# Performance work log

Measured on AMD Instinct MI355X. Metric: run time of the kernel, lower is better.

## Reference

```python
import jax, jax.numpy as jnp
import numpy as np

B, C_IN, T = 8, 1024, 4096
VQ_C, CODEBOOK, DS = 1024, 2048, 2


def setup_inputs() -> dict:
    key = jax.random.key(0)
    ks = jax.random.split(key, 6)
    return {
        "x": jax.random.normal(ks[0], (B, C_IN, T), jnp.float32),
        "x_mask": jnp.ones((B, 1, T), jnp.float32),
        "w_in": jax.random.normal(ks[1], (VQ_C, C_IN, DS), jnp.float32) * 0.02,
        "b_in": jnp.zeros((VQ_C,), jnp.float32),
        "embed": jax.random.normal(ks[2], (CODEBOOK, VQ_C), jnp.float32),
        "w_out": jax.random.normal(ks[3], (C_IN, VQ_C), jnp.float32) * 0.02,
        "b_out": jnp.zeros((C_IN,), jnp.float32),
    }


def reference(x, x_mask, w_in, b_in, embed, w_out, b_out):
    x_len = x.shape[2]
    ds = w_in.shape[-1]
    pad = (-x_len) % ds  # static under jit
    if pad:
        x = jnp.pad(x, ((0, 0), (0, 0), (0, pad)))
        x_mask = jnp.pad(x_mask, ((0, 0), (0, 0), (0, pad)))
    b, cin, tp = x.shape
    # conv_in: Conv1d(k=ds, stride=ds) == non-overlapping window contraction
    h = jnp.einsum('bcls,ocs->bol', x.reshape(b, cin, tp // ds, ds), w_in) + b_in[None, :, None]  # [B, D, L]
    tokens = h.transpose(0, 2, 1)  # [B, L, D]
    # euclidean codebook: ||t - e||^2 expanded (stable for argmin)
    d2 = (jnp.sum(tokens * tokens, -1, keepdims=True)
          - 2.0 * jnp.einsum('bld,nd->bln', tokens, embed)
          + jnp.sum(embed * embed, -1)[None, None, :])  # [B, L, N]
    idx = jnp.argmin(d2, axis=-1)  # [B, L]
    q = embed[idx]  # gather -> [B, L, D]
    # commitment loss (training-mode math; EMA codebook -> embed not a grad path)
    commit_loss = jnp.mean((jax.lax.stop_gradient(q) - tokens) ** 2)
    # straight-through estimator
    q_st = tokens + jax.lax.stop_gradient(q - tokens)
    q_cf = q_st.transpose(0, 2, 1)  # [B, D, L]
    # conv_out: nearest upsample x ds, then 1x1 conv
    up = jnp.repeat(q_cf, ds, axis=2)  # [B, D, Tp]
    out = jnp.einsum('bct,oc->bot', up, w_out) + b_out[None, :, None]
    out = out * x_mask
    return out[:, :, :x_len], commit_loss
```

## Files before the change

kernel.cpp:

```cpp
#include <hip/hip_runtime.h>

typedef _Float16 half8 __attribute__((ext_vector_type(8)));
typedef float f32x4 __attribute__((ext_vector_type(4)));

static constexpr int D = 1024;
static constexpr int NCODE = 2048;
static constexpr int MTOK = 16384;
static constexpr int KIN = 2048;
static constexpr int TLEN = 4096;
static constexpr int CAP = 2048;
#define TAU 0.4f

__device__ __forceinline__ void gload16(const void* g, void* l) {
  __builtin_amdgcn_global_load_lds(
      (const __attribute__((address_space(1))) void*)g,
      (__attribute__((address_space(3))) void*)l, 16, 0, 0);
}

#define SBAR()   asm volatile("s_barrier" ::: "memory")
#define WAITV4() asm volatile("s_waitcnt vmcnt(4)" ::: "memory")
#define WAITV0() asm volatile("s_waitcnt vmcnt(0)" ::: "memory")

__device__ __forceinline__ float key_to_f32(unsigned u) {
  unsigned bits = (u & 0x80000000u) ? (u & 0x7FFFFFFFu) : ~u;
  return __uint_as_float(bits);
}
__device__ __forceinline__ unsigned f32_to_key(float f) {
  unsigned ub = __float_as_uint(f);
  return (ub & 0x80000000u) ? ~ub : (ub | 0x80000000u);
}

__global__ __launch_bounds__(256) void k_pack_x(const float* __restrict__ x,
                                                _Float16* __restrict__ xh,
                                                _Float16* __restrict__ xl) {
  __shared__ float lds[32][65];
  const int tt0 = blockIdx.x * 64;
  const int cc0 = blockIdx.y * 32;
  const int b = blockIdx.z;
  const float* xb = x + ((size_t)b * D + cc0) * TLEN + tt0;
#pragma unroll
  for (int i = 0; i < 8; ++i) {
    int idx = threadIdx.x + i * 256;
    lds[idx >> 6][idx & 63] = xb[(size_t)(idx >> 6) * TLEN + (idx & 63)];
  }
  __syncthreads();
  const size_t mrow0 = (size_t)b * 2048 + (tt0 >> 1);
  const int r = threadIdx.x >> 3;
  const int g = threadIdx.x & 7;
  half8 vh, vl;
#pragma unroll
  for (int j = 0; j < 8; ++j) {
    int kk = g * 8 + j;
    float v = lds[kk >> 1][2 * r + (kk & 1)];
    _Float16 h = (_Float16)v;
    vh[j] = h;
    vl[j] = (_Float16)(v - (float)h);
  }
  size_t off = (mrow0 + r) * (size_t)KIN + (size_t)cc0 * 2 + g * 8;
  *(half8*)(xh + off) = vh;
  *(half8*)(xl + off) = vl;
}

__global__ __launch_bounds__(256) void k_split(const float* __restrict__ s,
                                               _Float16* __restrict__ hi,
                                               _Float16* __restrict__ lo, int n) {
  int i = blockIdx.x * 256 + threadIdx.x;
  if (i < n) {
    float v = s[i];
    _Float16 h = (_Float16)v;
    hi[i] = h;
    lo[i] = (_Float16)(v - (float)h);
  }
}

__global__ __launch_bounds__(256) void k_e2(const float* __restrict__ embed,
                                            float* __restrict__ e2c,
                                            int* __restrict__ counter,
                                            double* __restrict__ lossacc) {
  if (blockIdx.x == 0 && threadIdx.x == 0) { counter[0] = 0; lossacc[0] = 0.0; }
  int row = blockIdx.x * 4 + (threadIdx.x >> 6);
  int lane = threadIdx.x & 63;
  const float* er = embed + (size_t)row * D;
  double s = 0.0;
  for (int i = lane; i < D; i += 64) { double v = er[i]; s += v * v; }
#pragma unroll
  for (int mk = 1; mk < 64; mk <<= 1) s += __shfl_xor(s, mk, 64);
  if (lane == 0) e2c[row] = (float)(s - 1024.0);
}

template <int KDIM, int LOG_GX, int MODE>
__global__ __launch_bounds__(512, 2) void k_gemm_hh(
    const _Float16* __restrict__ Ah_, const _Float16* __restrict__ Bh_,
    const float* __restrict__ vec,
    _Float16* __restrict__ outh,
    unsigned long long* __restrict__ skKey, float* __restrict__ skSnd) {
  __shared__ _Float16 lds[3 * 16384];
  const int nwg = gridDim.x, bid = blockIdx.x, q = nwg >> 3;
  const int b2 = (bid & 7) * q + (bid >> 3);
  const int nb = b2 & ((1 << LOG_GX) - 1);
  const int n0 = nb * 256, m0 = (b2 >> LOG_GX) * 256;
  const int tid = threadIdx.x, lane = tid & 63, w = tid >> 6;
  const int wr = w >> 2, wc = w & 3, lr = lane & 15, lk = lane >> 4;
  constexpr int NT = KDIM / 32;
  const int cswz8 = (((lane & 3) ^ ((lane >> 3) & 3))) * 8;
  const int rswz8 = (lk ^ ((lr >> 1) & 3)) * 8;

  f32x4 acc[8][4] = {};

  auto stage = [&](int t, int c) {
    char* sb = (char*)(lds + c * 16384);
    const int k0 = t * 32;
    const int r0 = (w * 64 + lane) >> 2;
    gload16(Ah_ + (size_t)(m0 + r0) * KDIM + k0 + cswz8, sb + w * 1024);
    gload16(Ah_ + (size_t)(m0 + 128 + r0) * KDIM + k0 + cswz8, sb + w * 1024 + 8192);
    gload16(Bh_ + (size_t)(n0 + r0) * KDIM + k0 + cswz8, sb + 16384 + w * 1024);
    gload16(Bh_ + (size_t)(n0 + 128 + r0) * KDIM + k0 + cswz8, sb + 16384 + w * 1024 + 8192);
  };

  stage(0, 0);
  stage(1, 1);
  WAITV4();
  SBAR();

  int c0 = 0, c1 = 1, c2 = 2;
  for (int t = 0; t < NT; ++t) {
    const bool st = (t + 2) < NT;
    if (st) stage(t + 2, c2);
    const _Float16* sb = lds + c0 * 16384;
    half8 ah[8], bh[4];
#pragma unroll
    for (int f = 0; f < 8; ++f)
      ah[f] = *(const half8*)(sb + (wr * 128 + f * 16 + lr) * 32 + rswz8);
#pragma unroll
    for (int f = 0; f < 4; ++f)
      bh[f] = *(const half8*)(sb + 8192 + (wc * 64 + f * 16 + lr) * 32 + rswz8);
    __builtin_amdgcn_s_setprio(1);
#pragma unroll
    for (int fm = 0; fm < 8; ++fm)
#pragma unroll
      for (int fn = 0; fn < 4; ++fn)
        acc[fm][fn] = __builtin_amdgcn_mfma_f32_16x16x32_f16(ah[fm], bh[fn], acc[fm][fn], 0, 0, 0);
    __builtin_amdgcn_s_setprio(0);
    if (st) { WAITV4(); } else if (t + 1 < NT) { WAITV0(); }
    SBAR();
    int tmp = c0; c0 = c1; c1 = c2; c2 = tmp;
  }

  if constexpr (MODE == 0) {
#pragma unroll
    for (int fm = 0; fm < 8; ++fm) {
#pragma unroll
      for (int j = 0; j < 4; ++j) {
        int row = wr * 128 + fm * 16 + lk * 4 + j;
        size_t m = (size_t)m0 + row;
#pragma unroll
        for (int fn = 0; fn < 4; ++fn) {
          int col = n0 + wc * 64 + fn * 16 + lr;
          outh[m * (size_t)D + col] = (_Float16)(acc[fm][fn][j] + vec[col]);
        }
      }
    }
  } else {
#pragma unroll
    for (int fm = 0; fm < 8; ++fm) {
#pragma unroll
      for (int j = 0; j < 4; ++j) {
        int row = wr * 128 + fm * 16 + lk * 4 + j;
        size_t m = (size_t)m0 + row;
        float b1 = 3.4e38f, bb2 = 3.4e38f;
        int i1 = 0x7FFFFFFF;
#pragma unroll
        for (int fn = 0; fn < 4; ++fn) {
          int col = n0 + wc * 64 + fn * 16 + lr;
          float mv = vec[col] - 2.0f * acc[fm][fn][j];
          if (mv < b1) { bb2 = b1; b1 = mv; i1 = col; }
          else if (mv < bb2) { bb2 = mv; }
        }
#pragma unroll
        for (int mk = 1; mk < 16; mk <<= 1) {
          float ob1 = __shfl_xor(b1, mk, 64);
          float ob2 = __shfl_xor(bb2, mk, 64);
          int oi = __shfl_xor(i1, mk, 64);
          if (ob1 < b1) { bb2 = fminf(b1, ob2); b1 = ob1; i1 = oi; }
          else { bb2 = fminf(bb2, ob1); }
        }
        if (lr == 0) {
          unsigned long long key = ((unsigned long long)f32_to_key(b1) << 32) | (unsigned)i1;
          skKey[m * 32 + nb * 4 + wc] = key;
          skSnd[m * 32 + nb * 4 + wc] = bb2;
        }
      }
    }
  }
}

__global__ __launch_bounds__(256) void k_t2(const _Float16* __restrict__ tokh,
                                            float* __restrict__ t2) {
  const int w = threadIdx.x >> 6, lane = threadIdx.x & 63;
  const int row = blockIdx.x * 4 + w;
  const _Float16* tr = tokh + (size_t)row * D + lane * 16;
  float s = 0.f;
#pragma unroll
  for (int v = 0; v < 2; ++v) {
    half8 h = *(const half8*)(tr + v * 8);
#pragma unroll
    for (int j = 0; j < 8; ++j) { float f = (float)h[j]; s += f * f; }
  }
#pragma unroll
  for (int mk = 1; mk < 64; mk <<= 1) s += __shfl_xor(s, mk, 64);
  if (lane == 0) t2[row] = s;
}

__global__ __launch_bounds__(256) void k_flag(const unsigned long long* __restrict__ skKey,
                                              const float* __restrict__ skSnd,
                                              unsigned long long* __restrict__ keys,
                                              unsigned long long* __restrict__ keys2,
                                              int* __restrict__ list, int* __restrict__ counter) {
  int m = blockIdx.x * 256 + threadIdx.x;
  keys2[m] = ~0ull;
  unsigned long long best = ~0ull;
  int bsl = 0;
#pragma unroll
  for (int sl = 0; sl < 32; ++sl) {
    unsigned long long k = skKey[(size_t)m * 32 + sl];
    if (k < best) { best = k; bsl = sl; }
  }
  float b1 = key_to_f32((unsigned)(best >> 32));
  float second = skSnd[(size_t)m * 32 + bsl];
#pragma unroll
  for (int sl = 0; sl < 32; ++sl) {
    if (sl != bsl) second = fminf(second, key_to_f32((unsigned)(skKey[(size_t)m * 32 + sl] >> 32)));
  }
  keys[m] = best;
  if (second - b1 < TAU) {
    int p = atomicAdd(counter, 1);
    if (p < CAP) list[p] = m;
  }
}

__global__ __launch_bounds__(256) void k_tok_fix(
    const _Float16* __restrict__ xh, const _Float16* __restrict__ xl,
    const _Float16* __restrict__ wh, const _Float16* __restrict__ wl,
    const float* __restrict__ b_in, const int* __restrict__ list,
    const int* __restrict__ counter,
    _Float16* __restrict__ tokh2, _Float16* __restrict__ tokl2) {
  const int count = min(counter[0], CAP);
  const int m0 = blockIdx.y * 128;
  if (m0 >= count) return;
  __shared__ _Float16 sAh[128 * 32], sAl[128 * 32], sBh[128 * 32], sBl[128 * 32];
  const int n0 = blockIdx.x * 128;
  const int tid = threadIdx.x, lane = tid & 63, w = tid >> 6;
  const int wr = w >> 1, wc = w & 1, lr = lane & 15, lk = lane >> 4;
  f32x4 acc[4][4] = {};

  const int g0 = w * 128 + lane, g1 = g0 + 64;
  const int rA0 = g0 >> 2, cA0 = g0 & 3, rA1 = g1 >> 2, cA1 = g1 & 3;
  const int lb0 = (w * 128) * 16, lb1 = (w * 128 + 64) * 16;
  const int tk0 = list[min(m0 + rA0, count - 1)];
  const int tk1 = list[min(m0 + rA1, count - 1)];

  for (int kt = 0; kt < KIN / 32; ++kt) {
    const int k0 = kt * 32;
    gload16(xh + (size_t)tk0 * KIN + k0 + cA0 * 8, (char*)sAh + lb0);
    gload16(xh + (size_t)tk1 * KIN + k0 + cA1 * 8, (char*)sAh + lb1);
    gload16(xl + (size_t)tk0 * KIN + k0 + cA0 * 8, (char*)sAl + lb0);
    gload16(xl + (size_t)tk1 * KIN + k0 + cA1 * 8, (char*)sAl + lb1);
    gload16(wh + (size_t)(n0 + rA0) * KIN + k0 + cA0 * 8, (char*)sBh + lb0);
    gload16(wh + (size_t)(n0 + rA1) * KIN + k0 + cA1 * 8, (char*)sBh + lb1);
    gload16(wl + (size_t)(n0 + rA0) * KIN + k0 + cA0 * 8, (char*)sBl + lb0);
    gload16(wl + (size_t)(n0 + rA1) * KIN + k0 + cA1 * 8, (char*)sBl + lb1);
    __syncthreads();
    half8 ah[4], al2[4], bh[4], bl2[4];
#pragma unroll
    for (int f = 0; f < 4; ++f) {
      ah[f]  = *(const half8*)(sAh + (wr * 64 + f * 16 + lr) * 32 + lk * 8);
      al2[f] = *(const half8*)(sAl + (wr * 64 + f * 16 + lr) * 32 + lk * 8);
      bh[f]  = *(const half8*)(sBh + (wc * 64 + f * 16 + lr) * 32 + lk * 8);
      bl2[f] = *(const half8*)(sBl + (wc * 64 + f * 16 + lr) * 32 + lk * 8);
    }
#pragma unroll
    for (int fm = 0; fm < 4; ++fm)
#pragma unroll
      for (int fn = 0; fn < 4; ++fn) {
        acc[fm][fn] = __builtin_amdgcn_mfma_f32_16x16x32_f16(ah[fm], bh[fn], acc[fm][fn], 0, 0, 0);
        acc[fm][fn] = __builtin_amdgcn_mfma_f32_16x16x32_f16(ah[fm], bl2[fn], acc[fm][fn], 0, 0, 0);
        acc[fm][fn] = __builtin_amdgcn_mfma_f32_16x16x32_f16(al2[fm], bh[fn], acc[fm][fn], 0, 0, 0);
      }
    __syncthreads();
  }
#pragma unroll
  for (int fm = 0; fm < 4; ++fm) {
#pragma unroll
    for (int j = 0; j < 4; ++j) {
      int row = wr * 64 + fm * 16 + lk * 4 + j;
      if (m0 + row >= count) continue;
#pragma unroll
      for (int fn = 0; fn < 4; ++fn) {
        int col = n0 + wc * 64 + fn * 16 + lr;
        float v = acc[fm][fn][j] + b_in[col];
        _Float16 h = (_Float16)v;
        tokh2[(size_t)(m0 + row) * D + col] = h;
        tokl2[(size_t)(m0 + row) * D + col] = (_Float16)(v - (float)h);
      }
    }
  }
}

__global__ __launch_bounds__(256) void k_rescore(
    const _Float16* __restrict__ tokh2, const _Float16* __restrict__ tokl2,
    const _Float16* __restrict__ eh, const _Float16* __restrict__ el,
    const float* __restrict__ e2c, const int* __restrict__ list,
    const int* __restrict__ counter,
    unsigned long long* __restrict__ keys2) {
  const int count = min(counter[0], CAP);
  const int m0 = blockIdx.y * 128;
  if (m0 >= count) return;
  __shared__ _Float16 sAh[128 * 32], sAl[128 * 32], sBh[128 * 32], sBl[128 * 32];
  const int n0 = blockIdx.x * 128;
  const int tid = threadIdx.x, lane = tid & 63, w = tid >> 6;
  const int wr = w >> 1, wc = w & 1, lr = lane & 15, lk = lane >> 4;
  f32x4 acc[4][4] = {};

  const int g0 = w * 128 + lane, g1 = g0 + 64;
  const int rA0 = g0 >> 2, cA0 = g0 & 3, rA1 = g1 >> 2, cA1 = g1 & 3;
  const int lb0 = (w * 128) * 16, lb1 = (w * 128 + 64) * 16;

  for (int kt = 0; kt < D / 32; ++kt) {
    const int k0 = kt * 32;
    gload16(tokh2 + (size_t)(m0 + rA0) * D + k0 + cA0 * 8, (char*)sAh + lb0);
    gload16(tokh2 + (size_t)(m0 + rA1) * D + k0 + cA1 * 8, (char*)sAh + lb1);
    gload16(tokl2 + (size_t)(m0 + rA0) * D + k0 + cA0 * 8, (char*)sAl + lb0);
    gload16(tokl2 + (size_t)(m0 + rA1) * D + k0 + cA1 * 8, (char*)sAl + lb1);
    gload16(eh + (size_t)(n0 + rA0) * D + k0 + cA0 * 8, (char*)sBh + lb0);
    gload16(eh + (size_t)(n0 + rA1) * D + k0 + cA1 * 8, (char*)sBh + lb1);
    gload16(el + (size_t)(n0 + rA0) * D + k0 + cA0 * 8, (char*)sBl + lb0);
    gload16(el + (size_t)(n0 + rA1) * D + k0 + cA1 * 8, (char*)sBl + lb1);
    __syncthreads();
    half8 ah[4], al2[4], bh[4], bl2[4];
#pragma unroll
    for (int f = 0; f < 4; ++f) {
      ah[f]  = *(const half8*)(sAh + (wr * 64 + f * 16 + lr) * 32 + lk * 8);
      al2[f] = *(const half8*)(sAl + (wr * 64 + f * 16 + lr) * 32 + lk * 8);
      bh[f]  = *(const half8*)(sBh + (wc * 64 + f * 16 + lr) * 32 + lk * 8);
      bl2[f] = *(const half8*)(sBl + (wc * 64 + f * 16 + lr) * 32 + lk * 8);
    }
#pragma unroll
    for (int fm = 0; fm < 4; ++fm)
#pragma unroll
      for (int fn = 0; fn < 4; ++fn) {
        acc[fm][fn] = __builtin_amdgcn_mfma_f32_16x16x32_f16(ah[fm], bh[fn], acc[fm][fn], 0, 0, 0);
        acc[fm][fn] = __builtin_amdgcn_mfma_f32_16x16x32_f16(ah[fm], bl2[fn], acc[fm][fn], 0, 0, 0);
        acc[fm][fn] = __builtin_amdgcn_mfma_f32_16x16x32_f16(al2[fm], bh[fn], acc[fm][fn], 0, 0, 0);
      }
    __syncthreads();
  }
#pragma unroll
  for (int fm = 0; fm < 4; ++fm) {
#pragma unroll
    for (int j = 0; j < 4; ++j) {
      int row = wr * 64 + fm * 16 + lk * 4 + j;
      if (m0 + row >= count) continue;
      int tm = list[m0 + row];
      float best = 3.4e38f;
      int bidx = 0x7FFFFFFF;
#pragma unroll
      for (int fn = 0; fn < 4; ++fn) {
        int col = n0 + wc * 64 + fn * 16 + lr;
        float mv = e2c[col] - 2.0f * acc[fm][fn][j];
        if (mv < best) { best = mv; bidx = col; }
      }
#pragma unroll
      for (int mk = 1; mk < 16; mk <<= 1) {
        float ob = __shfl_xor(best, mk, 64);
        int oi = __shfl_xor(bidx, mk, 64);
        if (ob < best || (ob == best && oi < bidx)) { best = ob; bidx = oi; }
      }
      if (lr == 0) {
        unsigned long long key = ((unsigned long long)f32_to_key(best) << 32) | (unsigned)bidx;
        atomicMin(&keys2[tm], key);
      }
    }
  }
}

__global__ __launch_bounds__(256) void k_F(
    const _Float16* __restrict__ eh, const _Float16* __restrict__ el,
    const _Float16* __restrict__ woh, const _Float16* __restrict__ wol,
    const float* __restrict__ b_out, float* __restrict__ F) {
  __shared__ _Float16 sAh[128 * 32], sAl[128 * 32], sBh[128 * 32], sBl[128 * 32];
  const int n0 = blockIdx.x * 128, m0 = blockIdx.y * 128;
  const int tid = threadIdx.x, lane = tid & 63, w = tid >> 6;
  const int wr = w >> 1, wc = w & 1, lr = lane & 15, lk = lane >> 4;
  f32x4 acc[4][4] = {};

  const int g0 = w * 128 + lane, g1 = g0 + 64;
  const int rA0 = g0 >> 2, cA0 = g0 & 3, rA1 = g1 >> 2, cA1 = g1 & 3;
  const int lb0 = (w * 128) * 16, lb1 = (w * 128 + 64) * 16;

  for (int kt = 0; kt < D / 32; ++kt) {
    const int k0 = kt * 32;
    gload16(eh + (size_t)(m0 + rA0) * D + k0 + cA0 * 8, (char*)sAh + lb0);
    gload16(eh + (size_t)(m0 + rA1) * D + k0 + cA1 * 8, (char*)sAh + lb1);
    gload16(el + (size_t)(m0 + rA0) * D + k0 + cA0 * 8, (char*)sAl + lb0);
    gload16(el + (size_t)(m0 + rA1) * D + k0 + cA1 * 8, (char*)sAl + lb1);
    gload16(woh + (size_t)(n0 + rA0) * D + k0 + cA0 * 8, (char*)sBh + lb0);
    gload16(woh + (size_t)(n0 + rA1) * D + k0 + cA1 * 8, (char*)sBh + lb1);
    gload16(wol + (size_t)(n0 + rA0) * D + k0 + cA0 * 8, (char*)sBl + lb0);
    gload16(wol + (size_t)(n0 + rA1) * D + k0 + cA1 * 8, (char*)sBl + lb1);
    __syncthreads();
    half8 ah[4], al2[4], bh[4], bl2[4];
#pragma unroll
    for (int f = 0; f < 4; ++f) {
      ah[f]  = *(const half8*)(sAh + (wr * 64 + f * 16 + lr) * 32 + lk * 8);
      al2[f] = *(const half8*)(sAl + (wr * 64 + f * 16 + lr) * 32 + lk * 8);
      bh[f]  = *(const half8*)(sBh + (wc * 64 + f * 16 + lr) * 32 + lk * 8);
      bl2[f] = *(const half8*)(sBl + (wc * 64 + f * 16 + lr) * 32 + lk * 8);
    }
#pragma unroll
    for (int fm = 0; fm < 4; ++fm)
#pragma unroll
      for (int fn = 0; fn < 4; ++fn) {
        acc[fm][fn] = __builtin_amdgcn_mfma_f32_16x16x32_f16(ah[fm], bh[fn], acc[fm][fn], 0, 0, 0);
        acc[fm][fn] = __builtin_amdgcn_mfma_f32_16x16x32_f16(ah[fm], bl2[fn], acc[fm][fn], 0, 0, 0);
        acc[fm][fn] = __builtin_amdgcn_mfma_f32_16x16x32_f16(al2[fm], bh[fn], acc[fm][fn], 0, 0, 0);
      }
    __syncthreads();
  }
#pragma unroll
  for (int fm = 0; fm < 4; ++fm)
#pragma unroll
    for (int j = 0; j < 4; ++j) {
      int row = wr * 64 + fm * 16 + lk * 4 + j;
#pragma unroll
      for (int fn = 0; fn < 4; ++fn) {
        int col = n0 + wc * 64 + fn * 16 + lr;
        F[(size_t)(m0 + row) * D + col] = acc[fm][fn][j] + b_out[col];
      }
    }
}

__global__ __launch_bounds__(256) void k_expand(
    const float* __restrict__ F, const unsigned long long* __restrict__ keys,
    const unsigned long long* __restrict__ keys2,
    const float* __restrict__ mask, float* __restrict__ out) {
  __shared__ float ldsF[64 * 67];
  const int b = blockIdx.y;
  const int t0 = blockIdx.x * 128;
  const int ocbase = blockIdx.z * 512;
  const int tid = threadIdx.x;

  const int tok_w = tid & 63, ocr = tid >> 6;
  const float2 mv = *(const float2*)&mask[(size_t)b * TLEN + t0 + 2 * tok_w];
  float* outb = out + ((size_t)b * D) * TLEN + t0 + 2 * tok_w;

  const int ltk = tid >> 2, lg = tid & 3;
  const int lm = b * 2048 + (t0 >> 1) + ltk;
  unsigned long long kk = keys2[lm];
  if (kk == ~0ull) kk = keys[lm];
  const unsigned lidx = (unsigned)(kk & 0xFFFFFFFFull);
  const float* Fl = F + (size_t)lidx * D + lg * 16;

  for (int c8 = 0; c8 < 8; ++c8) {
    const int oc0 = ocbase + c8 * 64;
#pragma unroll
    for (int j = 0; j < 16; ++j)
      ldsF[ltk * 67 + lg * 16 + j] = Fl[oc0 + j];
    __syncthreads();
#pragma unroll
    for (int i = 0; i < 16; ++i) {
      int c = ocr + i * 4;
      float v = ldsF[tok_w * 67 + c];
      float2 o; o.x = v * mv.x; o.y = v * mv.y;
      *(float2*)&outb[(size_t)(oc0 + c) * TLEN] = o;
    }
    __syncthreads();
  }
}

__global__ __launch_bounds__(256) void k_loss(const unsigned long long* __restrict__ keys,
                                              const unsigned long long* __restrict__ keys2,
                                              const float* __restrict__ t2,
                                              double* __restrict__ acc) {
  int m = blockIdx.x * 256 + threadIdx.x;
  unsigned long long k = keys2[m];
  if (k == ~0ull) k = keys[m];
  float mval = key_to_f32((unsigned)(k >> 32));
  double c = (double)mval + 1024.0 + (double)t2[m];
#pragma unroll
  for (int mk = 1; mk < 64; mk <<= 1) c += __shfl_xor(c, mk, 64);
  __shared__ double part[4];
  if ((threadIdx.x & 63) == 0) part[threadIdx.x >> 6] = c;
  __syncthreads();
  if (threadIdx.x == 0) atomicAdd(acc, part[0] + part[1] + part[2] + part[3]);
}

__global__ void k_finalize(const double* __restrict__ acc, float* __restrict__ dst) {
  if (threadIdx.x == 0 && blockIdx.x == 0) *dst = (float)(*acc * (1.0 / 16777216.0));
}

extern "C" void kernel_launch(void* const* d_in, const int* in_sizes, int n_in,
                              void* d_out, int out_size, void* d_ws, size_t ws_size,
                              hipStream_t stream) {
  (void)in_sizes; (void)n_in; (void)out_size;
  const float* x      = (const float*)d_in[0];
  const float* xmask  = (const float*)d_in[1];
  const float* w_in   = (const float*)d_in[2];
  const float* b_in   = (const float*)d_in[3];
  const float* embed  = (const float*)d_in[4];
  const float* w_out  = (const float*)d_in[5];
  const float* b_out  = (const float*)d_in[6];
  float* out = (float*)d_out;

  _Float16* xh = (_Float16*)d_out;
  _Float16* xl = xh + (size_t)MTOK * KIN;

  char* p = (char*)d_ws;
  auto take = [&](size_t sz) { char* r = p; p += (sz + 255) & ~(size_t)255; return r; };
  _Float16* wh    = (_Float16*)take((size_t)D * KIN * 2);
  _Float16* wl    = (_Float16*)take((size_t)D * KIN * 2);
  _Float16* eh    = (_Float16*)take((size_t)NCODE * D * 2);
  _Float16* el    = (_Float16*)take((size_t)NCODE * D * 2);
  _Float16* woh   = (_Float16*)take((size_t)D * D * 2);
  _Float16* wol   = (_Float16*)take((size_t)D * D * 2);
  float* Fm       = (float*)take((size_t)NCODE * D * 4);
  float* e2c      = (float*)take((size_t)NCODE * 4);
  _Float16* tokh  = (_Float16*)take((size_t)MTOK * D * 2);
  _Float16* tokh2 = (_Float16*)take((size_t)CAP * D * 2);
  _Float16* tokl2 = (_Float16*)take((size_t)CAP * D * 2);
  float* t2       = (float*)take((size_t)MTOK * 4);
  unsigned long long* keys  = (unsigned long long*)take((size_t)MTOK * 8);
  unsigned long long* keys2 = (unsigned long long*)take((size_t)MTOK * 8);
  unsigned long long* skKey = (unsigned long long*)take((size_t)MTOK * 32 * 8);
  float* skSnd    = (float*)take((size_t)MTOK * 32 * 4);
  int* list       = (int*)take((size_t)CAP * 4);
  int* counter    = (int*)take(256);
  double* lossacc = (double*)take(256);
  if ((size_t)(p - (char*)d_ws) > ws_size) return;

  k_pack_x<<<dim3(64, 32, 8), 256, 0, stream>>>(x, xh, xl);
  k_split<<<(D * KIN + 255) / 256, 256, 0, stream>>>(w_in, wh, wl, D * KIN);
  k_split<<<(NCODE * D + 255) / 256, 256, 0, stream>>>(embed, eh, el, NCODE * D);
  k_split<<<(D * D + 255) / 256, 256, 0, stream>>>(w_out, woh, wol, D * D);
  k_e2<<<NCODE / 4, 256, 0, stream>>>(embed, e2c, counter, lossacc);

  k_F<<<dim3(D / 128, NCODE / 128), 256, 0, stream>>>(eh, el, woh, wol, b_out, Fm);

  k_gemm_hh<KIN, 2, 0><<<256, 512, 0, stream>>>(xh, wh, b_in, tokh, nullptr, nullptr);
  k_t2<<<MTOK / 4, 256, 0, stream>>>(tokh, t2);
  k_gemm_hh<D, 3, 1><<<512, 512, 0, stream>>>(tokh, eh, e2c, nullptr, skKey, skSnd);
  k_flag<<<MTOK / 256, 256, 0, stream>>>(skKey, skSnd, keys, keys2, list, counter);
  k_tok_fix<<<dim3(D / 128, CAP / 128), 256, 0, stream>>>(xh, xl, wh, wl, b_in, list, counter, tokh2, tokl2);
  k_rescore<<<dim3(NCODE / 128, CAP / 128), 256, 0, stream>>>(tokh2, tokl2, eh, el, e2c, list, counter, keys2);

  k_expand<<<dim3(TLEN / 128, 8, 2), 256, 0, stream>>>(Fm, keys, keys2, xmask, out);

  k_loss<<<MTOK / 256, 256, 0, stream>>>(keys, keys2, t2, lossacc);
  k_finalize<<<1, 64, 0, stream>>>(lossacc, out + (size_t)MTOK * KIN);
}
```

Baseline: 443.9 us.

## Fuse weight splits, fold token norms into GEMM epilogue, single-precision-half F GEMM

Merges the three hi/lo split launches into one kernel and drops the unused low half of w_out. The token squared-norm pass is folded into the conv_in GEMM epilogue: each row's partial sum is reduced across lanes and added to t2 with atomics, and t2 is zeroed in k_e2. This removes a separate read of the fp16 token matrix. The codebook-to-output F GEMM now uses only the fp16 high parts, cutting its MFMA work and loads to a third. The cost is lower precision in F and an order-dependent, nondeterministic atomic accumulation of t2.

```diff
diff --git a/kernel.cpp b/kernel.cpp
--- a/kernel.cpp
+++ b/kernel.cpp
@@ -61,23 +61,38 @@
   *(half8*)(xl + off) = vl;
 }
 
-__global__ __launch_bounds__(256) void k_split(const float* __restrict__ s,
-                                               _Float16* __restrict__ hi,
-                                               _Float16* __restrict__ lo, int n) {
+__global__ __launch_bounds__(256) void k_split3(
+    const float* __restrict__ w_in, const float* __restrict__ embed,
+    const float* __restrict__ w_out,
+    _Float16* __restrict__ wh, _Float16* __restrict__ wl,
+    _Float16* __restrict__ eh, _Float16* __restrict__ el,
+    _Float16* __restrict__ woh) {
   int i = blockIdx.x * 256 + threadIdx.x;
-  if (i < n) {
-    float v = s[i];
+  if (i < D * KIN) {
+    float v = w_in[i];
     _Float16 h = (_Float16)v;
-    hi[i] = h;
-    lo[i] = (_Float16)(v - (float)h);
+    wh[i] = h;
+    wl[i] = (_Float16)(v - (float)h);
+  } else if (i < D * KIN + NCODE * D) {
+    int j = i - D * KIN;
+    float v = embed[j];
+    _Float16 h = (_Float16)v;
+    eh[j] = h;
+    el[j] = (_Float16)(v - (float)h);
+  } else if (i < D * KIN + NCODE * D + D * D) {
+    int j = i - D * KIN - NCODE * D;
+    woh[j] = (_Float16)w_out[j];
   }
 }
 
 __global__ __launch_bounds__(256) void k_e2(const float* __restrict__ embed,
                                             float* __restrict__ e2c,
                                             int* __restrict__ counter,
-                                            double* __restrict__ lossacc) {
+                                            double* __restrict__ lossacc,
+                                            float* __restrict__ t2) {
   if (blockIdx.x == 0 && threadIdx.x == 0) { counter[0] = 0; lossacc[0] = 0.0; }
+  int g = blockIdx.x * 256 + threadIdx.x;
+  if (g < MTOK) t2[g] = 0.f;
   int row = blockIdx.x * 4 + (threadIdx.x >> 6);
   int lane = threadIdx.x & 63;
   const float* er = embed + (size_t)row * D;
@@ -92,7 +107,7 @@
 __global__ __launch_bounds__(512, 2) void k_gemm_hh(
     const _Float16* __restrict__ Ah_, const _Float16* __restrict__ Bh_,
     const float* __restrict__ vec,
-    _Float16* __restrict__ outh,
+    _Float16* __restrict__ outh, float* __restrict__ t2,
     unsigned long long* __restrict__ skKey, float* __restrict__ skSnd) {
   __shared__ _Float16 lds[3 * 16384];
   const int nwg = gridDim.x, bid = blockIdx.x, q = nwg >> 3;
@@ -153,11 +168,17 @@
       for (int j = 0; j < 4; ++j) {
         int row = wr * 128 + fm * 16 + lk * 4 + j;
         size_t m = (size_t)m0 + row;
+        float v2 = 0.f;
 #pragma unroll
         for (int fn = 0; fn < 4; ++fn) {
           int col = n0 + wc * 64 + fn * 16 + lr;
-          outh[m * (size_t)D + col] = (_Float16)(acc[fm][fn][j] + vec[col]);
+          float v = acc[fm][fn][j] + vec[col];
+          v2 += v * v;
+          outh[m * (size_t)D + col] = (_Float16)v;
         }
+#pragma unroll
+        for (int mk = 1; mk < 16; mk <<= 1) v2 += __shfl_xor(v2, mk, 64);
+        if (lr == 0) atomicAdd(&t2[m], v2);
       }
     }
   } else {
@@ -192,23 +213,6 @@
       }
     }
   }
-}
-
-__global__ __launch_bounds__(256) void k_t2(const _Float16* __restrict__ tokh,
-                                            float* __restrict__ t2) {
-  const int w = threadIdx.x >> 6, lane = threadIdx.x & 63;
-  const int row = blockIdx.x * 4 + w;
-  const _Float16* tr = tokh + (size_t)row * D + lane * 16;
-  float s = 0.f;
-#pragma unroll
-  for (int v = 0; v < 2; ++v) {
-    half8 h = *(const half8*)(tr + v * 8);
-#pragma unroll
-    for (int j = 0; j < 8; ++j) { float f = (float)h[j]; s += f * f; }
-  }
-#pragma unroll
-  for (int mk = 1; mk < 64; mk <<= 1) s += __shfl_xor(s, mk, 64);
-  if (lane == 0) t2[row] = s;
 }
 
 __global__ __launch_bounds__(256) void k_flag(const unsigned long long* __restrict__ skKey,
@@ -384,10 +388,9 @@
 }
 
 __global__ __launch_bounds__(256) void k_F(
-    const _Float16* __restrict__ eh, const _Float16* __restrict__ el,
-    const _Float16* __restrict__ woh, const _Float16* __restrict__ wol,
+    const _Float16* __restrict__ eh, const _Float16* __restrict__ woh,
     const float* __restrict__ b_out, float* __restrict__ F) {
-  __shared__ _Float16 sAh[128 * 32], sAl[128 * 32], sBh[128 * 32], sBl[128 * 32];
+  __shared__ _Float16 sA[128 * 32], sB[128 * 32];
   const int n0 = blockIdx.x * 128, m0 = blockIdx.y * 128;
   const int tid = threadIdx.x, lane = tid & 63, w = tid >> 6;
   const int wr = w >> 1, wc = w & 1, lr = lane & 15, lk = lane >> 4;
@@ -399,31 +402,22 @@
 
   for (int kt = 0; kt < D / 32; ++kt) {
     const int k0 = kt * 32;
-    gload16(eh + (size_t)(m0 + rA0) * D + k0 + cA0 * 8, (char*)sAh + lb0);
-    gload16(eh + (size_t)(m0 + rA1) * D + k0 + cA1 * 8, (char*)sAh + lb1);
-    gload16(el + (size_t)(m0 + rA0) * D + k0 + cA0 * 8, (char*)sAl + lb0);
-    gload16(el + (size_t)(m0 + rA1) * D + k0 + cA1 * 8, (char*)sAl + lb1);
-    gload16(woh + (size_t)(n0 + rA0) * D + k0 + cA0 * 8, (char*)sBh + lb0);
-    gload16(woh + (size_t)(n0 + rA1) * D + k0 + cA1 * 8, (char*)sBh + lb1);
-    gload16(wol + (size_t)(n0 + rA0) * D + k0 + cA0 * 8, (char*)sBl + lb0);
-    gload16(wol + (size_t)(n0 + rA1) * D + k0 + cA1 * 8, (char*)sBl + lb1);
-    __syncthreads();
-    half8 ah[4], al2[4], bh[4], bl2[4];
+    gload16(eh + (size_t)(m0 + rA0) * D + k0 + cA0 * 8, (char*)sA + lb0);
+    gload16(eh + (size_t)(m0 + rA1) * D + k0 + cA1 * 8, (char*)sA + lb1);
+    gload16(woh + (size_t)(n0 + rA0) * D + k0 + cA0 * 8, (char*)sB + lb0);
+    gload16(woh + (size_t)(n0 + rA1) * D + k0 + cA1 * 8, (char*)sB + lb1);
+    __syncthreads();
+    half8 a[4], b[4];
 #pragma unroll
     for (int f = 0; f < 4; ++f) {
-      ah[f]  = *(const half8*)(sAh + (wr * 64 + f * 16 + lr) * 32 + lk * 8);
-      al2[f] = *(const half8*)(sAl + (wr * 64 + f * 16 + lr) * 32 + lk * 8);
-      bh[f]  = *(const half8*)(sBh + (wc * 64 + f * 16 + lr) * 32 + lk * 8);
-      bl2[f] = *(const half8*)(sBl + (wc * 64 + f * 16 + lr) * 32 + lk * 8);
+      a[f] = *(const half8*)(sA + (wr * 64 + f * 16 + lr) * 32 + lk * 8);
+      b[f] = *(const half8*)(sB + (wc * 64 + f * 16 + lr) * 32 + lk * 8);
     }
 #pragma unroll
     for (int fm = 0; fm < 4; ++fm)
 #pragma unroll
-      for (int fn = 0; fn < 4; ++fn) {
-        acc[fm][fn] = __builtin_amdgcn_mfma_f32_16x16x32_f16(ah[fm], bh[fn], acc[fm][fn], 0, 0, 0);
-        acc[fm][fn] = __builtin_amdgcn_mfma_f32_16x16x32_f16(ah[fm], bl2[fn], acc[fm][fn], 0, 0, 0);
-        acc[fm][fn] = __builtin_amdgcn_mfma_f32_16x16x32_f16(al2[fm], bh[fn], acc[fm][fn], 0, 0, 0);
-      }
+      for (int fn = 0; fn < 4; ++fn)
+        acc[fm][fn] = __builtin_amdgcn_mfma_f32_16x16x32_f16(a[fm], b[fn], acc[fm][fn], 0, 0, 0);
     __syncthreads();
   }
 #pragma unroll
@@ -521,7 +515,6 @@
   _Float16* eh    = (_Float16*)take((size_t)NCODE * D * 2);
   _Float16* el    = (_Float16*)take((size_t)NCODE * D * 2);
   _Float16* woh   = (_Float16*)take((size_t)D * D * 2);
-  _Float16* wol   = (_Float16*)take((size_t)D * D * 2);
   float* Fm       = (float*)take((size_t)NCODE * D * 4);
   float* e2c      = (float*)take((size_t)NCODE * 4);
   _Float16* tokh  = (_Float16*)take((size_t)MTOK * D * 2);
@@ -538,16 +531,14 @@
   if ((size_t)(p - (char*)d_ws) > ws_size) return;
 
   k_pack_x<<<dim3(64, 32, 8), 256, 0, stream>>>(x, xh, xl);
-  k_split<<<(D * KIN + 255) / 256, 256, 0, stream>>>(w_in, wh, wl, D * KIN);
-  k_split<<<(NCODE * D + 255) / 256, 256, 0, stream>>>(embed, eh, el, NCODE * D);
-  k_split<<<(D * D + 255) / 256, 256, 0, stream>>>(w_out, woh, wol, D * D);
-  k_e2<<<NCODE / 4, 256, 0, stream>>>(embed, e2c, counter, lossacc);
-
-  k_F<<<dim3(D / 128, NCODE / 128), 256, 0, stream>>>(eh, el, woh, wol, b_out, Fm);
-
-  k_gemm_hh<KIN, 2, 0><<<256, 512, 0, stream>>>(xh, wh, b_in, tokh, nullptr, nullptr);
-  k_t2<<<MTOK / 4, 256, 0, stream>>>(tokh, t2);
-  k_gemm_hh<D, 3, 1><<<512, 512, 0, stream>>>(tokh, eh, e2c, nullptr, skKey, skSnd);
+  k_split3<<<(D * KIN + NCODE * D + D * D + 255) / 256, 256, 0, stream>>>(
+      w_in, embed, w_out, wh, wl, eh, el, woh);
+  k_e2<<<NCODE / 4, 256, 0, stream>>>(embed, e2c, counter, lossacc, t2);
+
+  k_F<<<dim3(D / 128, NCODE / 128), 256, 0, stream>>>(eh, woh, b_out, Fm);
+
+  k_gemm_hh<KIN, 2, 0><<<256, 512, 0, stream>>>(xh, wh, b_in, tokh, t2, nullptr, nullptr);
+  k_gemm_hh<D, 3, 1><<<512, 512, 0, stream>>>(tokh, eh, e2c, nullptr, nullptr, skKey, skSnd);
   k_flag<<<MTOK / 256, 256, 0, stream>>>(skKey, skSnd, keys, keys2, list, counter);
   k_tok_fix<<<dim3(D / 128, CAP / 128), 256, 0, stream>>>(xh, xl, wh, wl, b_in, list, counter, tokh2, tokl2);
   k_rescore<<<dim3(NCODE / 128, CAP / 128), 256, 0, stream>>>(tokh2, tokl2, eh, el, e2c, list, counter, keys2);
```

Measured after the change: 417.7 us (median of 2 runs). 1.06x faster.
